# Performance work log

Measured on AMD Instinct MI355X. Metric: run time of the kernel, lower is better.

## Reference

```python
import jax, jax.numpy as jnp
import numpy as np

K = 2          # number of strips per spatial axis
ALPHA = 0.5    # boost strength
BETA = 0.5     # suppression floor
EPS = 1e-5     # BatchNorm eps


def _strip_attn(fm, w, b, gamma, beta, mean, var, axis):
    """1x1 conv (C->1) + BN(eval) + ReLU, per-strip avgpool along `axis`,
    softmax over the K strips, broadcast back to full resolution.
    fm: [B, C, W, H]; returns attention of shape [B, W] (axis=2) or [B, H] (axis=3)."""
    B, C, W, H = fm.shape
    conv = jnp.einsum('bcwh,c->bwh', fm, w) + b[0]          # [B, W, H]
    bn = (conv - mean[0]) * (gamma[0] / jnp.sqrt(var[0] + EPS)) + beta[0]
    act = jax.nn.relu(bn)
    if axis == 2:
        # strips along W: [B, K, W//K, H] -> mean over strip
        pooled = act.reshape(B, K, W // K, H).mean(axis=(2, 3))   # [B, K]
        rep = W // K
    else:
        # strips along H: [B, W, K, H//K] -> mean over strip
        pooled = act.reshape(B, W, K, H // K).mean(axis=(1, 3))   # [B, K]
        rep = W // K  # original code uses w // k for both repeats (w == h here)
    attn = jax.nn.softmax(pooled, axis=1)                     # [B, K]
    return jnp.repeat(attn, rep, axis=1)                      # [B, W] or [B, H]


def reference(fm, w_w, b_w, gamma_w, beta_w, mean_w, var_w,
              w_h, b_h, gamma_h, beta_h, mean_h, var_h):
    aw = _strip_attn(fm, w_w, b_w, gamma_w, beta_w, mean_w, var_w, axis=2)  # [B, W]
    ah = _strip_attn(fm, w_h, b_h, gamma_h, beta_h, mean_h, var_h, axis=3)  # [B, H]
    # fm_final: [B, 1, W, H] (broadcast over channels)
    fm_final = aw[:, None, :, None] * ah[:, None, None, :]
    fms_boost = fm + ALPHA * (fm * fm_final)
    # per-sample max over fm_final; suppress mask = 1.0 where below 0.95*max, else BETA
    fms_max = fm_final.max(axis=(1, 2, 3), keepdims=True)                   # [B,1,1,1]
    mask = jnp.where(fm_final < fms_max * 0.95, jnp.float32(1.0), jnp.float32(BETA))
    fms_suppress = fm * mask
    return fms_boost, fms_suppress


def setup_inputs() -> dict:
    key = jax.random.key(0)
    k1, k2, k3 = jax.random.split(key, 3)
    B, C, W, H = 32, 1024, 32, 32
    fan_out = 1  # kaiming fan_out for 1x1 conv with 1 output channel -> std = sqrt(2/1)
    std = float(np.sqrt(2.0 / 1.0))
    return {
        'fm': jax.random.normal(k1, (B, C, W, H), dtype=jnp.float32),
        'w_w': jax.random.normal(k2, (C,), dtype=jnp.float32) * std,
        'b_w': jnp.zeros((1,), jnp.float32),
        'gamma_w': jnp.ones((1,), jnp.float32),
        'beta_w': jnp.zeros((1,), jnp.float32),
        'mean_w': jnp.zeros((1,), jnp.float32),
        'var_w': jnp.ones((1,), jnp.float32),
        'w_h': jax.random.normal(k3, (C,), dtype=jnp.float32) * std,
        'b_h': jnp.zeros((1,), jnp.float32),
        'gamma_h': jnp.ones((1,), jnp.float32),
        'beta_h': jnp.zeros((1,), jnp.float32),
        'mean_h': jnp.zeros((1,), jnp.float32),
        'var_h': jnp.ones((1,), jnp.float32),
    }
```

## Files before the change

kernel.cpp:

```cpp
#include <hip/hip_runtime.h>

#define BN_EPS 1e-5f
#define ALPHA 0.5f
#define BETA 0.5f


typedef float vfloat4 __attribute__((ext_vector_type(4)));

__global__ __launch_bounds__(256) void k_conv(
    const float* __restrict__ fm, const float* __restrict__ wW,
    const float* __restrict__ wH, const float* __restrict__ bw,
    const float* __restrict__ gw, const float* __restrict__ betw,
    const float* __restrict__ mw, const float* __restrict__ vw,
    const float* __restrict__ bh, const float* __restrict__ gh,
    const float* __restrict__ beth, const float* __restrict__ mh,
    const float* __restrict__ vh, float* __restrict__ pooled_w,
    float* __restrict__ pooled_h) {
  __shared__ float lw[1024];
  __shared__ float lh[1024];
  __shared__ float4 part_w[32][8];
  __shared__ float4 part_h[32][8];

  const int t = threadIdx.x;
  const int b = blockIdx.x >> 5;
  const int row = blockIdx.x & 31;

  {
    const float4 a = reinterpret_cast<const float4*>(wW)[t];
    const float4 c = reinterpret_cast<const float4*>(wH)[t];
    reinterpret_cast<float4*>(lw)[t] = a;
    reinterpret_cast<float4*>(lh)[t] = c;
  }
  __syncthreads();

  const int c_off = t >> 3;
  const int s4 = t & 7;
  const float4* f4 = reinterpret_cast<const float4*>(fm) +
                     ((size_t)(b * 1024 + c_off) * 256 + row * 8 + s4);

  float4 aw = {0.f, 0.f, 0.f, 0.f};
  float4 ah = {0.f, 0.f, 0.f, 0.f};
#pragma unroll 8
  for (int it = 0; it < 32; ++it) {
    const int c = it * 32 + c_off;
    const float4 v = f4[(size_t)it * 32 * 256];
    const float sw = lw[c];
    const float sh = lh[c];
    aw.x = fmaf(v.x, sw, aw.x);
    aw.y = fmaf(v.y, sw, aw.y);
    aw.z = fmaf(v.z, sw, aw.z);
    aw.w = fmaf(v.w, sw, aw.w);
    ah.x = fmaf(v.x, sh, ah.x);
    ah.y = fmaf(v.y, sh, ah.y);
    ah.z = fmaf(v.z, sh, ah.z);
    ah.w = fmaf(v.w, sh, ah.w);
  }
  part_w[c_off][s4] = aw;
  part_h[c_off][s4] = ah;
  __syncthreads();

  if (t < 8) {
    const float scale_w = gw[0] * rsqrtf(vw[0] + BN_EPS);
    const float shift_w = (bw[0] - mw[0]) * scale_w + betw[0];
    const float scale_h = gh[0] * rsqrtf(vh[0] + BN_EPS);
    const float shift_h = (bh[0] - mh[0]) * scale_h + beth[0];

    float4 cw = {0.f, 0.f, 0.f, 0.f};
    float4 ch = {0.f, 0.f, 0.f, 0.f};
#pragma unroll
    for (int g = 0; g < 32; ++g) {
      const float4 pw = part_w[g][t];
      const float4 ph = part_h[g][t];
      cw.x += pw.x; cw.y += pw.y; cw.z += pw.z; cw.w += pw.w;
      ch.x += ph.x; ch.y += ph.y; ch.z += ph.z; ch.w += ph.w;
    }
    float aws = fmaxf(fmaf(cw.x, scale_w, shift_w), 0.f) +
                fmaxf(fmaf(cw.y, scale_w, shift_w), 0.f) +
                fmaxf(fmaf(cw.z, scale_w, shift_w), 0.f) +
                fmaxf(fmaf(cw.w, scale_w, shift_w), 0.f);
    float ahs = fmaxf(fmaf(ch.x, scale_h, shift_h), 0.f) +
                fmaxf(fmaf(ch.y, scale_h, shift_h), 0.f) +
                fmaxf(fmaf(ch.z, scale_h, shift_h), 0.f) +
                fmaxf(fmaf(ch.w, scale_h, shift_h), 0.f);
    const int kh = (t >> 2) & 1;
    float v0 = kh == 0 ? ahs : 0.f;
    float v1 = kh == 1 ? ahs : 0.f;
#pragma unroll
    for (int off = 4; off >= 1; off >>= 1) {
      aws += __shfl_xor(aws, off);
      v0 += __shfl_xor(v0, off);
      v1 += __shfl_xor(v1, off);
    }
    if (t == 0) {
      const int kw = row >> 4;
      atomicAdd(&pooled_w[b * 2 + kw], aws);
      atomicAdd(&pooled_h[b * 2 + 0], v0);
      atomicAdd(&pooled_h[b * 2 + 1], v1);
    }
  }
}

__global__ __launch_bounds__(64) void k_factors(
    const float* __restrict__ pooled_w, const float* __restrict__ pooled_h,
    float2* __restrict__ fac) {
  const int b = threadIdx.x;
  if (b >= 32) return;
  const float pw0 = pooled_w[b * 2 + 0] * (1.f / 512.f);
  const float pw1 = pooled_w[b * 2 + 1] * (1.f / 512.f);
  const float ph0 = pooled_h[b * 2 + 0] * (1.f / 512.f);
  const float ph1 = pooled_h[b * 2 + 1] * (1.f / 512.f);

  const float mwv = fmaxf(pw0, pw1);
  const float ew0 = __expf(pw0 - mwv), ew1 = __expf(pw1 - mwv);
  const float sw0 = ew0 / (ew0 + ew1), sw1 = ew1 / (ew0 + ew1);
  const float mhv = fmaxf(ph0, ph1);
  const float eh0 = __expf(ph0 - mhv), eh1 = __expf(ph1 - mhv);
  const float sh0 = eh0 / (eh0 + eh1), sh1 = eh1 / (eh0 + eh1);

  float f[4];
  f[0] = sw0 * sh0;
  f[1] = sw0 * sh1;
  f[2] = sw1 * sh0;
  f[3] = sw1 * sh1;
  const float thr = fmaxf(fmaxf(f[0], f[1]), fmaxf(f[2], f[3])) * 0.95f;
#pragma unroll
  for (int q = 0; q < 4; ++q) {
    const float boost = 1.f + ALPHA * f[q];
    const float mask = (f[q] < thr) ? 1.f : BETA;
    fac[b * 4 + q] = make_float2(boost, mask);
  }
}

__global__ __launch_bounds__(256) void k_out(
    const float* __restrict__ fm, const float2* __restrict__ fac,
    float* __restrict__ out0, float* __restrict__ out1) {
  const size_t i0 = (size_t)blockIdx.x * 256 + threadIdx.x;
  const vfloat4* fm4 = reinterpret_cast<const vfloat4*>(fm);
  vfloat4* o0 = reinterpret_cast<vfloat4*>(out0);
  vfloat4* o1 = reinterpret_cast<vfloat4*>(out1);
#pragma unroll
  for (int k = 0; k < 4; ++k) {
    const size_t i = i0 + (size_t)k * 2097152;
    const size_t e = i * 4;
    const int b = (int)(e >> 20);
    const int kw = ((int)(e >> 5) & 31) >> 4;
    const int kh = ((int)e & 31) >> 4;
    const float2 f = fac[(b << 2) | (kw << 1) | kh];
    const vfloat4 v = fm4[i];
    __builtin_nontemporal_store(v * f.x, &o0[i]);
    __builtin_nontemporal_store(v * f.y, &o1[i]);
  }
}

extern "C" void kernel_launch(void* const* d_in, const int* in_sizes, int n_in,
                              void* d_out, int out_size, void* d_ws,
                              size_t ws_size, hipStream_t stream) {
  const float* fm = (const float*)d_in[0];
  const float* w_w = (const float*)d_in[1];
  const float* b_w = (const float*)d_in[2];
  const float* g_w = (const float*)d_in[3];
  const float* be_w = (const float*)d_in[4];
  const float* m_w = (const float*)d_in[5];
  const float* v_w = (const float*)d_in[6];
  const float* w_h = (const float*)d_in[7];
  const float* b_h = (const float*)d_in[8];
  const float* g_h = (const float*)d_in[9];
  const float* be_h = (const float*)d_in[10];
  const float* m_h = (const float*)d_in[11];
  const float* v_h = (const float*)d_in[12];

  float* ws = (float*)d_ws;
  float* pooled_w = ws;
  float* pooled_h = ws + 64;
  float2* fac = (float2*)(ws + 128);

  float* out0 = (float*)d_out;
  float* out1 = out0 + (size_t)32 * 1024 * 1024;

  hipMemsetAsync(d_ws, 0, 128 * sizeof(float), stream);

  k_conv<<<32 * 32, 256, 0, stream>>>(fm, w_w, w_h, b_w, g_w, be_w, m_w, v_w,
                                      b_h, g_h, be_h, m_h, v_h, pooled_w,
                                      pooled_h);
  k_factors<<<1, 64, 0, stream>>>(pooled_w, pooled_h, fac);
  k_out<<<8192, 256, 0, stream>>>(fm, fac, out0, out1);
}
```

Measured before the change: 102.5 us.

## Split batch into halves so the output pass rereads fm from cache

The work is now done in two batch halves of 16 samples, each running conv, reduction and output back to back. The aim is for k_out to reread that half's 64MB of fm while it is still resident in the large last-level cache rather than fetching it again from HBM. The conv kernel is reorganised to write per-channel-chunk partial sums to workspace with no atomics or memset, and a new k_mid kernel reduces those partials and computes the factors. The cost is six launches instead of three, a 16-block mid kernel that leaves most of the GPU idle, and 8MB of extra partial-sum traffic.

```diff
diff --git a/kernel.cpp b/kernel.cpp
--- a/kernel.cpp
+++ b/kernel.cpp
@@ -9,138 +9,115 @@
 
 __global__ __launch_bounds__(256) void k_conv(
     const float* __restrict__ fm, const float* __restrict__ wW,
-    const float* __restrict__ wH, const float* __restrict__ bw,
-    const float* __restrict__ gw, const float* __restrict__ betw,
-    const float* __restrict__ mw, const float* __restrict__ vw,
-    const float* __restrict__ bh, const float* __restrict__ gh,
-    const float* __restrict__ beth, const float* __restrict__ mh,
-    const float* __restrict__ vh, float* __restrict__ pooled_w,
-    float* __restrict__ pooled_h) {
-  __shared__ float lw[1024];
-  __shared__ float lh[1024];
-  __shared__ float4 part_w[32][8];
-  __shared__ float4 part_h[32][8];
-
+    const float* __restrict__ wH, float* __restrict__ part_w,
+    float* __restrict__ part_h, int b0) {
+  const int blk = blockIdx.x;
+  const int bl = blk >> 6;
+  const int ch = blk & 63;
   const int t = threadIdx.x;
-  const int b = blockIdx.x >> 5;
-  const int row = blockIdx.x & 31;
-
-  {
-    const float4 a = reinterpret_cast<const float4*>(wW)[t];
-    const float4 c = reinterpret_cast<const float4*>(wH)[t];
-    reinterpret_cast<float4*>(lw)[t] = a;
-    reinterpret_cast<float4*>(lh)[t] = c;
+  const vfloat4* f4 = reinterpret_cast<const vfloat4*>(fm) +
+                      ((size_t)((b0 + bl) * 1024 + ch * 16) * 256 + t);
+  vfloat4 aw = {0.f, 0.f, 0.f, 0.f};
+  vfloat4 ah = {0.f, 0.f, 0.f, 0.f};
+#pragma unroll
+  for (int c = 0; c < 16; ++c) {
+    const vfloat4 v = f4[(size_t)c * 256];
+    const float sw = wW[ch * 16 + c];
+    const float sh = wH[ch * 16 + c];
+    aw += v * sw;
+    ah += v * sh;
   }
-  __syncthreads();
-
-  const int c_off = t >> 3;
-  const int s4 = t & 7;
-  const float4* f4 = reinterpret_cast<const float4*>(fm) +
-                     ((size_t)(b * 1024 + c_off) * 256 + row * 8 + s4);
-
-  float4 aw = {0.f, 0.f, 0.f, 0.f};
-  float4 ah = {0.f, 0.f, 0.f, 0.f};
-#pragma unroll 8
-  for (int it = 0; it < 32; ++it) {
-    const int c = it * 32 + c_off;
-    const float4 v = f4[(size_t)it * 32 * 256];
-    const float sw = lw[c];
-    const float sh = lh[c];
-    aw.x = fmaf(v.x, sw, aw.x);
-    aw.y = fmaf(v.y, sw, aw.y);
-    aw.z = fmaf(v.z, sw, aw.z);
-    aw.w = fmaf(v.w, sw, aw.w);
-    ah.x = fmaf(v.x, sh, ah.x);
-    ah.y = fmaf(v.y, sh, ah.y);
-    ah.z = fmaf(v.z, sh, ah.z);
-    ah.w = fmaf(v.w, sh, ah.w);
-  }
-  part_w[c_off][s4] = aw;
-  part_h[c_off][s4] = ah;
-  __syncthreads();
-
-  if (t < 8) {
-    const float scale_w = gw[0] * rsqrtf(vw[0] + BN_EPS);
-    const float shift_w = (bw[0] - mw[0]) * scale_w + betw[0];
-    const float scale_h = gh[0] * rsqrtf(vh[0] + BN_EPS);
-    const float shift_h = (bh[0] - mh[0]) * scale_h + beth[0];
-
-    float4 cw = {0.f, 0.f, 0.f, 0.f};
-    float4 ch = {0.f, 0.f, 0.f, 0.f};
-#pragma unroll
-    for (int g = 0; g < 32; ++g) {
-      const float4 pw = part_w[g][t];
-      const float4 ph = part_h[g][t];
-      cw.x += pw.x; cw.y += pw.y; cw.z += pw.z; cw.w += pw.w;
-      ch.x += ph.x; ch.y += ph.y; ch.z += ph.z; ch.w += ph.w;
-    }
-    float aws = fmaxf(fmaf(cw.x, scale_w, shift_w), 0.f) +
-                fmaxf(fmaf(cw.y, scale_w, shift_w), 0.f) +
-                fmaxf(fmaf(cw.z, scale_w, shift_w), 0.f) +
-                fmaxf(fmaf(cw.w, scale_w, shift_w), 0.f);
-    float ahs = fmaxf(fmaf(ch.x, scale_h, shift_h), 0.f) +
-                fmaxf(fmaf(ch.y, scale_h, shift_h), 0.f) +
-                fmaxf(fmaf(ch.z, scale_h, shift_h), 0.f) +
-                fmaxf(fmaf(ch.w, scale_h, shift_h), 0.f);
-    const int kh = (t >> 2) & 1;
-    float v0 = kh == 0 ? ahs : 0.f;
-    float v1 = kh == 1 ? ahs : 0.f;
-#pragma unroll
-    for (int off = 4; off >= 1; off >>= 1) {
-      aws += __shfl_xor(aws, off);
-      v0 += __shfl_xor(v0, off);
-      v1 += __shfl_xor(v1, off);
-    }
-    if (t == 0) {
-      const int kw = row >> 4;
-      atomicAdd(&pooled_w[b * 2 + kw], aws);
-      atomicAdd(&pooled_h[b * 2 + 0], v0);
-      atomicAdd(&pooled_h[b * 2 + 1], v1);
-    }
-  }
+  const int o = (bl * 64 + ch) * 256 + t;
+  reinterpret_cast<vfloat4*>(part_w)[o] = aw;
+  reinterpret_cast<vfloat4*>(part_h)[o] = ah;
 }
 
-__global__ __launch_bounds__(64) void k_factors(
-    const float* __restrict__ pooled_w, const float* __restrict__ pooled_h,
-    float2* __restrict__ fac) {
-  const int b = threadIdx.x;
-  if (b >= 32) return;
-  const float pw0 = pooled_w[b * 2 + 0] * (1.f / 512.f);
-  const float pw1 = pooled_w[b * 2 + 1] * (1.f / 512.f);
-  const float ph0 = pooled_h[b * 2 + 0] * (1.f / 512.f);
-  const float ph1 = pooled_h[b * 2 + 1] * (1.f / 512.f);
+__global__ __launch_bounds__(256) void k_mid(
+    const float* __restrict__ part_w, const float* __restrict__ part_h,
+    const float* __restrict__ bw, const float* __restrict__ gw,
+    const float* __restrict__ betw, const float* __restrict__ mw,
+    const float* __restrict__ vw, const float* __restrict__ bh,
+    const float* __restrict__ gh, const float* __restrict__ beth,
+    const float* __restrict__ mh, const float* __restrict__ vh,
+    float2* __restrict__ fac, int b0) {
+  __shared__ vfloat4 red[4];
+  const int bl = blockIdx.x;
+  const int t = threadIdx.x;
+  const vfloat4* pw4 =
+      reinterpret_cast<const vfloat4*>(part_w) + bl * 16384 + t;
+  const vfloat4* ph4 =
+      reinterpret_cast<const vfloat4*>(part_h) + bl * 16384 + t;
+  vfloat4 cw = {0.f, 0.f, 0.f, 0.f};
+  vfloat4 chv = {0.f, 0.f, 0.f, 0.f};
+#pragma unroll 8
+  for (int k = 0; k < 64; ++k) {
+    cw += pw4[k * 256];
+    chv += ph4[k * 256];
+  }
+  const float scale_w = gw[0] * rsqrtf(vw[0] + BN_EPS);
+  const float shift_w = (bw[0] - mw[0]) * scale_w + betw[0];
+  const float scale_h = gh[0] * rsqrtf(vh[0] + BN_EPS);
+  const float shift_h = (bh[0] - mh[0]) * scale_h + beth[0];
 
-  const float mwv = fmaxf(pw0, pw1);
-  const float ew0 = __expf(pw0 - mwv), ew1 = __expf(pw1 - mwv);
-  const float sw0 = ew0 / (ew0 + ew1), sw1 = ew1 / (ew0 + ew1);
-  const float mhv = fmaxf(ph0, ph1);
-  const float eh0 = __expf(ph0 - mhv), eh1 = __expf(ph1 - mhv);
-  const float sh0 = eh0 / (eh0 + eh1), sh1 = eh1 / (eh0 + eh1);
-
-  float f[4];
-  f[0] = sw0 * sh0;
-  f[1] = sw0 * sh1;
-  f[2] = sw1 * sh0;
-  f[3] = sw1 * sh1;
-  const float thr = fmaxf(fmaxf(f[0], f[1]), fmaxf(f[2], f[3])) * 0.95f;
+  const float aws = fmaxf(fmaf(cw.x, scale_w, shift_w), 0.f) +
+                    fmaxf(fmaf(cw.y, scale_w, shift_w), 0.f) +
+                    fmaxf(fmaf(cw.z, scale_w, shift_w), 0.f) +
+                    fmaxf(fmaf(cw.w, scale_w, shift_w), 0.f);
+  const float ahs = fmaxf(fmaf(chv.x, scale_h, shift_h), 0.f) +
+                    fmaxf(fmaf(chv.y, scale_h, shift_h), 0.f) +
+                    fmaxf(fmaf(chv.z, scale_h, shift_h), 0.f) +
+                    fmaxf(fmaf(chv.w, scale_h, shift_h), 0.f);
+  const int kw = t >> 7;
+  const int kh = (t & 7) >> 2;
+  vfloat4 s;
+  s.x = kw ? 0.f : aws;
+  s.y = kw ? aws : 0.f;
+  s.z = kh ? 0.f : ahs;
+  s.w = kh ? ahs : 0.f;
 #pragma unroll
-  for (int q = 0; q < 4; ++q) {
-    const float boost = 1.f + ALPHA * f[q];
-    const float mask = (f[q] < thr) ? 1.f : BETA;
-    fac[b * 4 + q] = make_float2(boost, mask);
+  for (int off = 32; off >= 1; off >>= 1) {
+    s.x += __shfl_xor(s.x, off);
+    s.y += __shfl_xor(s.y, off);
+    s.z += __shfl_xor(s.z, off);
+    s.w += __shfl_xor(s.w, off);
+  }
+  if ((t & 63) == 0) red[t >> 6] = s;
+  __syncthreads();
+  if (t == 0) {
+    const vfloat4 a = red[0] + red[1] + red[2] + red[3];
+    const float pw0 = a.x * (1.f / 512.f), pw1 = a.y * (1.f / 512.f);
+    const float ph0 = a.z * (1.f / 512.f), ph1 = a.w * (1.f / 512.f);
+    const float mwv = fmaxf(pw0, pw1);
+    const float ew0 = __expf(pw0 - mwv), ew1 = __expf(pw1 - mwv);
+    const float sw0 = ew0 / (ew0 + ew1), sw1 = ew1 / (ew0 + ew1);
+    const float mhv = fmaxf(ph0, ph1);
+    const float eh0 = __expf(ph0 - mhv), eh1 = __expf(ph1 - mhv);
+    const float sh0 = eh0 / (eh0 + eh1), sh1 = eh1 / (eh0 + eh1);
+    float f[4];
+    f[0] = sw0 * sh0;
+    f[1] = sw0 * sh1;
+    f[2] = sw1 * sh0;
+    f[3] = sw1 * sh1;
+    const float thr = fmaxf(fmaxf(f[0], f[1]), fmaxf(f[2], f[3])) * 0.95f;
+#pragma unroll
+    for (int q = 0; q < 4; ++q) {
+      fac[(b0 + bl) * 4 + q] =
+          make_float2(1.f + ALPHA * f[q], (f[q] < thr) ? 1.f : BETA);
+    }
   }
 }
 
 __global__ __launch_bounds__(256) void k_out(
     const float* __restrict__ fm, const float2* __restrict__ fac,
-    float* __restrict__ out0, float* __restrict__ out1) {
+    float* __restrict__ out0, float* __restrict__ out1, int b0) {
+  const size_t base = (size_t)b0 << 18;
   const size_t i0 = (size_t)blockIdx.x * 256 + threadIdx.x;
   const vfloat4* fm4 = reinterpret_cast<const vfloat4*>(fm);
   vfloat4* o0 = reinterpret_cast<vfloat4*>(out0);
   vfloat4* o1 = reinterpret_cast<vfloat4*>(out1);
 #pragma unroll
   for (int k = 0; k < 4; ++k) {
-    const size_t i = i0 + (size_t)k * 2097152;
+    const size_t i = base + i0 + (size_t)k * 1048576;
     const size_t e = i * 4;
     const int b = (int)(e >> 20);
     const int kw = ((int)(e >> 5) & 31) >> 4;
@@ -170,18 +147,18 @@
   const float* v_h = (const float*)d_in[12];
 
   float* ws = (float*)d_ws;
-  float* pooled_w = ws;
-  float* pooled_h = ws + 64;
-  float2* fac = (float2*)(ws + 128);
+  float* part_w = ws;
+  float* part_h = ws + (1 << 20);
+  float2* fac = (float2*)(ws + (1 << 21));
 
   float* out0 = (float*)d_out;
   float* out1 = out0 + (size_t)32 * 1024 * 1024;
 
-  hipMemsetAsync(d_ws, 0, 128 * sizeof(float), stream);
-
-  k_conv<<<32 * 32, 256, 0, stream>>>(fm, w_w, w_h, b_w, g_w, be_w, m_w, v_w,
-                                      b_h, g_h, be_h, m_h, v_h, pooled_w,
-                                      pooled_h);
-  k_factors<<<1, 64, 0, stream>>>(pooled_w, pooled_h, fac);
-  k_out<<<8192, 256, 0, stream>>>(fm, fac, out0, out1);
+  for (int g = 0; g < 2; ++g) {
+    const int b0 = g * 16;
+    k_conv<<<1024, 256, 0, stream>>>(fm, w_w, w_h, part_w, part_h, b0);
+    k_mid<<<16, 256, 0, stream>>>(part_w, part_h, b_w, g_w, be_w, m_w, v_w,
+                                  b_h, g_h, be_h, m_h, v_h, fac, b0);
+    k_out<<<4096, 256, 0, stream>>>(fm, fac, out0, out1, b0);
+  }
 }
```

Result: slower. 115.3 us (+12.5%).

## Fuse softmax factor kernel into conv via last-block counter, reverse output traversal

Applied to the files above, without the earlier changes.

Removes the separate single-block factor kernel: each batch's last conv block, detected with an agent-scope acq_rel atomic counter, computes the softmax/boost/mask factors itself. The output kernel now uses fewer blocks that each loop over 16 segments in reverse order, likely so the most recently read tail of fm is reused from cache. It also switches from nontemporal to normal stores. This saves one launch and may improve L2/MALL hits, at the cost of atomics plus a larger memset.

```diff
diff --git a/kernel.cpp b/kernel.cpp
--- a/kernel.cpp
+++ b/kernel.cpp
@@ -6,6 +6,7 @@
 
 
 typedef float vfloat4 __attribute__((ext_vector_type(4)));
+#define SCOPE_AGENT __HIP_MEMORY_SCOPE_AGENT
 
 __global__ __launch_bounds__(256) void k_conv(
     const float* __restrict__ fm, const float* __restrict__ wW,
@@ -15,7 +16,8 @@
     const float* __restrict__ bh, const float* __restrict__ gh,
     const float* __restrict__ beth, const float* __restrict__ mh,
     const float* __restrict__ vh, float* __restrict__ pooled_w,
-    float* __restrict__ pooled_h) {
+    float* __restrict__ pooled_h, unsigned int* __restrict__ cnt,
+    float2* __restrict__ fac) {
   __shared__ float lw[1024];
   __shared__ float lh[1024];
   __shared__ float4 part_w[32][8];
@@ -26,37 +28,27 @@
   const int row = blockIdx.x & 31;
 
   {
-    const float4 a = reinterpret_cast<const float4*>(wW)[t];
-    const float4 c = reinterpret_cast<const float4*>(wH)[t];
-    reinterpret_cast<float4*>(lw)[t] = a;
-    reinterpret_cast<float4*>(lh)[t] = c;
+    reinterpret_cast<float4*>(lw)[t] = reinterpret_cast<const float4*>(wW)[t];
+    reinterpret_cast<float4*>(lh)[t] = reinterpret_cast<const float4*>(wH)[t];
   }
   __syncthreads();
 
   const int c_off = t >> 3;
   const int s4 = t & 7;
-  const float4* f4 = reinterpret_cast<const float4*>(fm) +
-                     ((size_t)(b * 1024 + c_off) * 256 + row * 8 + s4);
+  const vfloat4* f4 = reinterpret_cast<const vfloat4*>(fm) +
+                      ((size_t)(b * 1024 + c_off) * 256 + row * 8 + s4);
 
-  float4 aw = {0.f, 0.f, 0.f, 0.f};
-  float4 ah = {0.f, 0.f, 0.f, 0.f};
+  vfloat4 aw = {0.f, 0.f, 0.f, 0.f};
+  vfloat4 ah = {0.f, 0.f, 0.f, 0.f};
 #pragma unroll 8
   for (int it = 0; it < 32; ++it) {
     const int c = it * 32 + c_off;
-    const float4 v = f4[(size_t)it * 32 * 256];
-    const float sw = lw[c];
-    const float sh = lh[c];
-    aw.x = fmaf(v.x, sw, aw.x);
-    aw.y = fmaf(v.y, sw, aw.y);
-    aw.z = fmaf(v.z, sw, aw.z);
-    aw.w = fmaf(v.w, sw, aw.w);
-    ah.x = fmaf(v.x, sh, ah.x);
-    ah.y = fmaf(v.y, sh, ah.y);
-    ah.z = fmaf(v.z, sh, ah.z);
-    ah.w = fmaf(v.w, sh, ah.w);
+    const vfloat4 v = f4[(size_t)it * 32 * 256];
+    aw += v * lw[c];
+    ah += v * lh[c];
   }
-  part_w[c_off][s4] = aw;
-  part_h[c_off][s4] = ah;
+  part_w[c_off][s4] = (float4){aw.x, aw.y, aw.z, aw.w};
+  part_h[c_off][s4] = (float4){ah.x, ah.y, ah.z, ah.w};
   __syncthreads();
 
   if (t < 8) {
@@ -78,11 +70,11 @@
                 fmaxf(fmaf(cw.y, scale_w, shift_w), 0.f) +
                 fmaxf(fmaf(cw.z, scale_w, shift_w), 0.f) +
                 fmaxf(fmaf(cw.w, scale_w, shift_w), 0.f);
-    float ahs = fmaxf(fmaf(ch.x, scale_h, shift_h), 0.f) +
-                fmaxf(fmaf(ch.y, scale_h, shift_h), 0.f) +
-                fmaxf(fmaf(ch.z, scale_h, shift_h), 0.f) +
-                fmaxf(fmaf(ch.w, scale_h, shift_h), 0.f);
-    const int kh = (t >> 2) & 1;
+    const float ahs = fmaxf(fmaf(ch.x, scale_h, shift_h), 0.f) +
+                      fmaxf(fmaf(ch.y, scale_h, shift_h), 0.f) +
+                      fmaxf(fmaf(ch.z, scale_h, shift_h), 0.f) +
+                      fmaxf(fmaf(ch.w, scale_h, shift_h), 0.f);
+    const int kh = t >> 2;
     float v0 = kh == 0 ? ahs : 0.f;
     float v1 = kh == 1 ? ahs : 0.f;
 #pragma unroll
@@ -96,59 +88,61 @@
       atomicAdd(&pooled_w[b * 2 + kw], aws);
       atomicAdd(&pooled_h[b * 2 + 0], v0);
       atomicAdd(&pooled_h[b * 2 + 1], v1);
+      const unsigned int old = __hip_atomic_fetch_add(
+          &cnt[b * 16], 1u, __ATOMIC_ACQ_REL, SCOPE_AGENT);
+      if (old == 31u) {
+        const float pw0 = __hip_atomic_load(&pooled_w[b * 2 + 0],
+                                            __ATOMIC_RELAXED, SCOPE_AGENT) *
+                          (1.f / 512.f);
+        const float pw1 = __hip_atomic_load(&pooled_w[b * 2 + 1],
+                                            __ATOMIC_RELAXED, SCOPE_AGENT) *
+                          (1.f / 512.f);
+        const float ph0 = __hip_atomic_load(&pooled_h[b * 2 + 0],
+                                            __ATOMIC_RELAXED, SCOPE_AGENT) *
+                          (1.f / 512.f);
+        const float ph1 = __hip_atomic_load(&pooled_h[b * 2 + 1],
+                                            __ATOMIC_RELAXED, SCOPE_AGENT) *
+                          (1.f / 512.f);
+        const float mwv = fmaxf(pw0, pw1);
+        const float ew0 = __expf(pw0 - mwv), ew1 = __expf(pw1 - mwv);
+        const float sw0 = ew0 / (ew0 + ew1), sw1 = ew1 / (ew0 + ew1);
+        const float mhv = fmaxf(ph0, ph1);
+        const float eh0 = __expf(ph0 - mhv), eh1 = __expf(ph1 - mhv);
+        const float sh0 = eh0 / (eh0 + eh1), sh1 = eh1 / (eh0 + eh1);
+        float f[4];
+        f[0] = sw0 * sh0;
+        f[1] = sw0 * sh1;
+        f[2] = sw1 * sh0;
+        f[3] = sw1 * sh1;
+        const float thr =
+            fmaxf(fmaxf(f[0], f[1]), fmaxf(f[2], f[3])) * 0.95f;
+#pragma unroll
+        for (int q = 0; q < 4; ++q) {
+          fac[b * 4 + q] =
+              make_float2(1.f + ALPHA * f[q], (f[q] < thr) ? 1.f : BETA);
+        }
+      }
     }
-  }
-}
-
-__global__ __launch_bounds__(64) void k_factors(
-    const float* __restrict__ pooled_w, const float* __restrict__ pooled_h,
-    float2* __restrict__ fac) {
-  const int b = threadIdx.x;
-  if (b >= 32) return;
-  const float pw0 = pooled_w[b * 2 + 0] * (1.f / 512.f);
-  const float pw1 = pooled_w[b * 2 + 1] * (1.f / 512.f);
-  const float ph0 = pooled_h[b * 2 + 0] * (1.f / 512.f);
-  const float ph1 = pooled_h[b * 2 + 1] * (1.f / 512.f);
-
-  const float mwv = fmaxf(pw0, pw1);
-  const float ew0 = __expf(pw0 - mwv), ew1 = __expf(pw1 - mwv);
-  const float sw0 = ew0 / (ew0 + ew1), sw1 = ew1 / (ew0 + ew1);
-  const float mhv = fmaxf(ph0, ph1);
-  const float eh0 = __expf(ph0 - mhv), eh1 = __expf(ph1 - mhv);
-  const float sh0 = eh0 / (eh0 + eh1), sh1 = eh1 / (eh0 + eh1);
-
-  float f[4];
-  f[0] = sw0 * sh0;
-  f[1] = sw0 * sh1;
-  f[2] = sw1 * sh0;
-  f[3] = sw1 * sh1;
-  const float thr = fmaxf(fmaxf(f[0], f[1]), fmaxf(f[2], f[3])) * 0.95f;
-#pragma unroll
-  for (int q = 0; q < 4; ++q) {
-    const float boost = 1.f + ALPHA * f[q];
-    const float mask = (f[q] < thr) ? 1.f : BETA;
-    fac[b * 4 + q] = make_float2(boost, mask);
   }
 }
 
 __global__ __launch_bounds__(256) void k_out(
     const float* __restrict__ fm, const float2* __restrict__ fac,
     float* __restrict__ out0, float* __restrict__ out1) {
-  const size_t i0 = (size_t)blockIdx.x * 256 + threadIdx.x;
+  const int t = threadIdx.x;
   const vfloat4* fm4 = reinterpret_cast<const vfloat4*>(fm);
   vfloat4* o0 = reinterpret_cast<vfloat4*>(out0);
   vfloat4* o1 = reinterpret_cast<vfloat4*>(out1);
-#pragma unroll
-  for (int k = 0; k < 4; ++k) {
-    const size_t i = i0 + (size_t)k * 2097152;
-    const size_t e = i * 4;
-    const int b = (int)(e >> 20);
-    const int kw = ((int)(e >> 5) & 31) >> 4;
-    const int kh = ((int)e & 31) >> 4;
-    const float2 f = fac[(b << 2) | (kw << 1) | kh];
+#pragma unroll 4
+  for (int c = 0; c < 16; ++c) {
+    const int seg = 32767 - (c * 2048 + (int)blockIdx.x);
+    const size_t i = (size_t)seg * 256 + t;
+    const int idx = (((int)(i >> 18)) << 2) | ((((int)i >> 7) & 1) << 1) |
+                    (((int)i >> 2) & 1);
+    const float2 f = fac[idx];
     const vfloat4 v = fm4[i];
-    __builtin_nontemporal_store(v * f.x, &o0[i]);
-    __builtin_nontemporal_store(v * f.y, &o1[i]);
+    o0[i] = v * f.x;
+    o1[i] = v * f.y;
   }
 }
 
@@ -169,19 +163,19 @@
   const float* m_h = (const float*)d_in[11];
   const float* v_h = (const float*)d_in[12];
 
-  float* ws = (float*)d_ws;
-  float* pooled_w = ws;
-  float* pooled_h = ws + 64;
-  float2* fac = (float2*)(ws + 128);
+  char* ws = (char*)d_ws;
+  float* pooled_w = (float*)(ws + 0);
+  float* pooled_h = (float*)(ws + 256);
+  unsigned int* cnt = (unsigned int*)(ws + 512);
+  float2* fac = (float2*)(ws + 2560);
 
   float* out0 = (float*)d_out;
   float* out1 = out0 + (size_t)32 * 1024 * 1024;
 
-  hipMemsetAsync(d_ws, 0, 128 * sizeof(float), stream);
+  hipMemsetAsync(d_ws, 0, 2560, stream);
 
   k_conv<<<32 * 32, 256, 0, stream>>>(fm, w_w, w_h, b_w, g_w, be_w, m_w, v_w,
                                       b_h, g_h, be_h, m_h, v_h, pooled_w,
-                                      pooled_h);
-  k_factors<<<1, 64, 0, stream>>>(pooled_w, pooled_h, fac);
-  k_out<<<8192, 256, 0, stream>>>(fm, fac, out0, out1);
+                                      pooled_h, cnt, fac);
+  k_out<<<2048, 256, 0, stream>>>(fm, fac, out0, out1);
 }
```

Result: slower. 152.6 us (+48.8%).
